# Kernel optimization log

Hardware: AMD Instinct MI355X
Metric: run time of the kernel (lower is better)

The kernel has to match this reference:

```python
import jax, jax.numpy as jnp
import numpy as np

B, S, D_IN, D_OUT = 4, 2048, 1024, 1024

def setup_inputs() -> dict:
    key = jax.random.key(0)
    k1, k2, k3, k4 = jax.random.split(key, 4)
    x = jax.random.normal(k1, (B, S, D_IN), dtype=jnp.float32)
    # nn.Linear(d_in, d_out, bias=False): y = x @ W.T with W [d_out, d_in].
    # We store the transposed [d_in, d_out] matrices directly.
    Wq = jax.random.normal(k2, (D_IN, D_OUT), dtype=jnp.float32) * (1.0 / np.sqrt(D_IN))
    Wk = jax.random.normal(k3, (D_IN, D_OUT), dtype=jnp.float32) * (1.0 / np.sqrt(D_IN))
    Wv = jax.random.normal(k4, (D_IN, D_OUT), dtype=jnp.float32) * (1.0 / np.sqrt(D_IN))
    return {"x": x, "Wq": Wq, "Wk": Wk, "Wv": Wv}

def reference(x, Wq, Wk, Wv):
    b, num_tokens, d_in = x.shape
    q = jnp.einsum('bsd,de->bse', x, Wq)
    k = jnp.einsum('bsd,de->bse', x, Wk)
    v = jnp.einsum('bsd,de->bse', x, Wv)
    scale = 1.0 / jnp.sqrt(jnp.asarray(k.shape[-1], dtype=x.dtype))
    scores = jnp.einsum('bqe,bke->bqk', q, k)  # [b, S, S]
    causal = jnp.tril(jnp.ones((num_tokens, num_tokens), dtype=bool))
    scores = jnp.where(causal[None, :, :], scores, -jnp.inf)
    attn = jax.nn.softmax(scores * scale, axis=-1)
    # dropout p=0.0 (eval/deterministic): identity
    return jnp.einsum('bqk,bke->bqe', attn, v)
```

## Files before the change

### kernel.cpp

```cpp
#include <hip/hip_runtime.h>

typedef unsigned short u16;
typedef unsigned int u32;
typedef __attribute__((ext_vector_type(8))) __bf16 bf16x8;
typedef __attribute__((ext_vector_type(4))) float f32x4;
typedef __attribute__((ext_vector_type(4))) u16 u16x4;

#define DEVFN static __device__ __forceinline__

constexpr int S_ = 2048;
constexpr int D_ = 1024;
constexpr float SCALE_ = 0.03125f;

DEVFN u16 f2bf(float f) {
  u32 u = __builtin_bit_cast(u32, f);
  return (u16)((u + 0x7fffu + ((u >> 16) & 1u)) >> 16);
}
DEVFN float bf2f(u16 h) {
  u32 u = ((u32)h) << 16;
  return __builtin_bit_cast(float, u);
}
DEVFN void gld16(const u16* g, u16* l) {
  __builtin_amdgcn_global_load_lds(
      (const __attribute__((address_space(1))) u32*)g,
      (__attribute__((address_space(3))) u32*)l, 16, 0, 0);
}

__global__ __launch_bounds__(256) void cvt_x_kernel(const float* __restrict__ x,
                                                    u16* __restrict__ xb) {
  int i = blockIdx.x * 256 + threadIdx.x;
  float4 v = ((const float4*)x)[i];
  u16x4 o = {f2bf(v.x), f2bf(v.y), f2bf(v.z), f2bf(v.w)};
  ((u16x4*)xb)[i] = o;
}

__global__ __launch_bounds__(256) void transpose_w_kernel(const float* __restrict__ W,
                                                          u16* __restrict__ Wt) {
  __shared__ float t[32][33];
  int tx = threadIdx.x, ty = threadIdx.y;
  int n0 = blockIdx.x * 32, k0 = blockIdx.y * 32;
#pragma unroll
  for (int i = 0; i < 4; ++i)
    t[ty + i * 8][tx] = W[(size_t)(k0 + ty + i * 8) * D_ + n0 + tx];
  __syncthreads();
#pragma unroll
  for (int i = 0; i < 4; ++i)
    Wt[(size_t)(n0 + ty + i * 8) * D_ + k0 + tx] = f2bf(t[tx][ty + i * 8]);
}

__global__ __launch_bounds__(256) void reduce_mt_kernel(const float* __restrict__ P4,
                                                        u16* __restrict__ Mt) {
  int i = (blockIdx.x * 256 + threadIdx.x) * 4;
  float4 a = *(const float4*)(P4 + i);
  float4 b = *(const float4*)(P4 + 1048576 + i);
  float4 c = *(const float4*)(P4 + 2097152 + i);
  float4 d = *(const float4*)(P4 + 3145728 + i);
  u16x4 o = {f2bf(a.x + b.x + c.x + d.x), f2bf(a.y + b.y + c.y + d.y),
             f2bf(a.z + b.z + c.z + d.z), f2bf(a.w + b.w + c.w + d.w)};
  *(u16x4*)(Mt + i) = o;
}

__global__ __launch_bounds__(512, 2) void gemm256(const u16* __restrict__ A,
                                                  const u16* __restrict__ Bt,
                                                  u16* __restrict__ O0,
                                                  u16* __restrict__ O2) {
  int tm = blockIdx.x, tn = blockIdx.y;
  constexpr int LDA = 1024, LDB = 1024;
  const int NKT = 32;

  __shared__ u16 ls[4][2][8192];

  int tid = threadIdx.x;
  int lane = tid & 63, wid = tid >> 6;
  int wm = wid >> 2, wn = wid & 3;

  const u16* Ab = A + (size_t)tm * 256 * LDA;
  const u16* Bb = Bt + (size_t)tn * 256 * LDB;

  int gsw = tid ^ ((tid >> 3) & 7);
  int srow = gsw >> 2;
  int scol = (gsw & 3) * 8;

#define STAGE(bf, kt)                                                           \
  do {                                                                          \
    int k0_ = (kt) * 32;                                                        \
    gld16(Ab + (size_t)srow * LDA + k0_ + scol, &ls[bf][0][0] + tid * 8);       \
    gld16(Ab + (size_t)(srow + 128) * LDA + k0_ + scol,                         \
          &ls[bf][0][0] + 4096 + tid * 8);                                      \
    gld16(Bb + (size_t)srow * LDB + k0_ + scol, &ls[bf][1][0] + tid * 8);       \
    gld16(Bb + (size_t)(srow + 128) * LDB + k0_ + scol,                         \
          &ls[bf][1][0] + 4096 + tid * 8);                                      \
  } while (0)

  const int kg_ = lane >> 4;
  const int arow = wm * 128 + (lane & 15);
  const int brow = wn * 64 + (lane & 15);
  const int aoff = ((arow * 4 + kg_) ^ ((arow >> 1) & 7)) * 8;
  const int boff = ((brow * 4 + kg_) ^ ((brow >> 1) & 7)) * 8;

  f32x4 acc[8][4] = {};

  STAGE(0, 0);
  STAGE(1, 1);
  STAGE(2, 2);

#define KSTEP(t, W)                                                             \
  do {                                                                          \
    asm volatile("s_waitcnt vmcnt(%0)" ::"n"(W) : "memory");                    \
    __builtin_amdgcn_s_barrier();                                               \
    __builtin_amdgcn_sched_barrier(0);                                          \
    if ((t) + 3 < NKT) STAGE(((t) + 3) & 3, (t) + 3);                           \
    const u16* la_ = &ls[(t) & 3][0][0] + aoff;                                 \
    const u16* lb_ = &ls[(t) & 3][1][0] + boff;                                 \
    bf16x8 aF[8], bF[4];                                                        \
    _Pragma("unroll") for (int f = 0; f < 8; ++f)                               \
        aF[f] = *(const bf16x8*)(la_ + f * 512);                                \
    _Pragma("unroll") for (int f = 0; f < 4; ++f)                               \
        bF[f] = *(const bf16x8*)(lb_ + f * 512);                                \
    __builtin_amdgcn_s_setprio(1);                                              \
    _Pragma("unroll") for (int fm = 0; fm < 8; ++fm)                            \
        _Pragma("unroll") for (int fn = 0; fn < 4; ++fn)                        \
            acc[fm][fn] = __builtin_amdgcn_mfma_f32_16x16x32_bf16(              \
                aF[fm], bF[fn], acc[fm][fn], 0, 0, 0);                          \
    __builtin_amdgcn_s_setprio(0);                                              \
  } while (0)

  for (int t = 0; t < NKT - 2; ++t) KSTEP(t, 8);
  KSTEP(NKT - 2, 4);
  KSTEP(NKT - 1, 0);

#undef KSTEP
#undef STAGE

  int r0 = tm * 256 + wm * 128 + (lane >> 4) * 4;
  int c0 = tn * 256 + wn * 64 + (lane & 15);

  if (tn < 4) {
#pragma unroll
    for (int fm = 0; fm < 8; ++fm)
#pragma unroll
      for (int fn = 0; fn < 4; ++fn)
#pragma unroll
        for (int i = 0; i < 4; ++i)
          O0[(size_t)(r0 + fm * 16 + i) * 1024 + (c0 + fn * 16)] =
              f2bf(acc[fm][fn][i]);
  } else {
#pragma unroll
    for (int fm = 0; fm < 8; ++fm)
#pragma unroll
      for (int fn = 0; fn < 4; ++fn) {
        int r = r0 + fm * 16;
        int bb = r >> 11, s0 = r & 2047;
        int e = c0 + fn * 16 - 1024;
        u16x4 o = {f2bf(acc[fm][fn][0]), f2bf(acc[fm][fn][1]),
                   f2bf(acc[fm][fn][2]), f2bf(acc[fm][fn][3])};
        *(u16x4*)(O2 + (size_t)bb * 2097152 + (size_t)e * 2048 + s0) = o;
      }
  }
}

template <int MODE, int NBUF>
__global__ __launch_bounds__(256, NBUF == 3 ? 3 : 2) void
gemm128(const u16* __restrict__ A, const u16* __restrict__ Bt,
        u16* __restrict__ O0, float* __restrict__ OF) {
  int tm, tn, z;
  if (MODE == 3) {
    int id = blockIdx.x;
    tn = id & 7;
    z = (id >> 3) & 3;
    int tmh = id >> 5;
    tm = (tmh < 8) ? tmh : 23 - tmh;
  } else if (MODE == 2) {
    int id = blockIdx.x;
    z = id & 3;
    int tri = id >> 2;
    int r = (int)((sqrtf(8.0f * (float)tri + 1.0f) - 1.0f) * 0.5f);
    while ((r + 1) * (r + 2) / 2 <= tri) ++r;
    while (r * (r + 1) / 2 > tri) --r;
    tm = r;
    tn = tri - r * (r + 1) / 2;
  } else {
    tm = blockIdx.x;
    tn = blockIdx.y;
    z = blockIdx.z;
  }
  constexpr int LDA = (MODE == 3) ? 2048 : 1024;
  constexpr int LDB = (MODE == 3) ? 2048 : 1024;
  const int NKT = (MODE == 3) ? (tm + 1) * 4 : (MODE == 4 ? 8 : 32);

  __shared__ u16 ls[NBUF][2][4096];

  int tid = threadIdx.x;
  int lane = tid & 63, wid = tid >> 6;
  int wm = wid >> 1, wn = wid & 1;

  const u16* Ab = A +
      (MODE == 2 ? (size_t)z * (2048 * 1024)
                 : (MODE == 3 ? (size_t)z * (2048 * 2048) : (size_t)0)) +
      (MODE == 4 ? z * 256 : 0) + (size_t)tm * 128 * LDA;
  const u16* Bb = Bt +
      (MODE == 2 ? (size_t)z * (2048 * 1024)
                 : (MODE == 3 ? (size_t)z * (1024 * 2048) : (size_t)0)) +
      (MODE == 4 ? z * 256 : 0) + (size_t)tn * 128 * LDB;

  int gsw = tid ^ ((tid >> 3) & 7);
  int sr = gsw >> 2;
  int sc = (gsw & 3) * 8;

#define STG(bf, kt)                                                             \
  do {                                                                          \
    int k0_ = (kt) * 32;                                                        \
    gld16(Ab + (size_t)sr * LDA + k0_ + sc, &ls[bf][0][0] + tid * 8);           \
    gld16(Ab + (size_t)(sr + 64) * LDA + k0_ + sc,                              \
          &ls[bf][0][0] + 2048 + tid * 8);                                      \
    gld16(Bb + (size_t)sr * LDB + k0_ + sc, &ls[bf][1][0] + tid * 8);           \
    gld16(Bb + (size_t)(sr + 64) * LDB + k0_ + sc,                              \
          &ls[bf][1][0] + 2048 + tid * 8);                                      \
  } while (0)

  const int kg_ = lane >> 4;
  const int arow = wm * 64 + (lane & 15);
  const int brow = wn * 64 + (lane & 15);
  const int aoff = ((arow * 4 + kg_) ^ ((arow >> 1) & 7)) * 8;
  const int boff = ((brow * 4 + kg_) ^ ((brow >> 1) & 7)) * 8;

  f32x4 acc[4][4] = {};
  int rb = 0, wb = 2;

  STG(0, 0);
  STG(1, 1);
  if (NBUF == 4) STG(2, 2);

#define KSTEP(t, W)                                                             \
  do {                                                                          \
    asm volatile("s_waitcnt vmcnt(%0)" ::"n"(W) : "memory");                    \
    __builtin_amdgcn_s_barrier();                                               \
    __builtin_amdgcn_sched_barrier(0);                                          \
    if (NBUF == 4) {                                                            \
      if ((t) + 3 < NKT) STG(((t) + 3) & 3, (t) + 3);                           \
    } else {                                                                    \
      if ((t) + 2 < NKT) STG(wb, (t) + 2);                                      \
    }                                                                           \
    const u16* la_ = &ls[(NBUF == 4) ? ((t) & 3) : rb][0][0] + aoff;            \
    const u16* lb_ = &ls[(NBUF == 4) ? ((t) & 3) : rb][1][0] + boff;            \
    bf16x8 aF[4], bF[4];                                                        \
    _Pragma("unroll") for (int f = 0; f < 4; ++f)                               \
        aF[f] = *(const bf16x8*)(la_ + f * 512);                                \
    _Pragma("unroll") for (int f = 0; f < 4; ++f)                               \
        bF[f] = *(const bf16x8*)(lb_ + f * 512);                                \
    __builtin_amdgcn_s_setprio(1);                                              \
    _Pragma("unroll") for (int fm = 0; fm < 4; ++fm)                            \
        _Pragma("unroll") for (int fn = 0; fn < 4; ++fn)                        \
            acc[fm][fn] = __builtin_amdgcn_mfma_f32_16x16x32_bf16(              \
                aF[fm], bF[fn], acc[fm][fn], 0, 0, 0);                          \
    __builtin_amdgcn_s_setprio(0);                                              \
    if (NBUF == 3) {                                                            \
      rb = (rb == 2) ? 0 : rb + 1;                                              \
      wb = (wb == 2) ? 0 : wb + 1;                                              \
    }                                                                           \
  } while (0)

  if (NBUF == 4) {
    for (int t = 0; t < NKT - 2; ++t) KSTEP(t, 8);
    KSTEP(NKT - 2, 4);
    KSTEP(NKT - 1, 0);
  } else {
    for (int t = 0; t < NKT - 1; ++t) KSTEP(t, 4);
    KSTEP(NKT - 1, 0);
  }

#undef KSTEP
#undef STG

  int r0 = tm * 128 + wm * 64 + (lane >> 4) * 4;
  int c0 = tn * 128 + wn * 64 + (lane & 15);

  if (MODE == 2) {
    u16* P = O0 + (size_t)z * 4194304;
#pragma unroll
    for (int fm = 0; fm < 4; ++fm)
#pragma unroll
      for (int fn = 0; fn < 4; ++fn)
#pragma unroll
        for (int i = 0; i < 4; ++i)
          P[(size_t)(r0 + fm * 16 + i) * 2048 + (c0 + fn * 16)] =
              f2bf(acc[fm][fn][i]);
  } else if (MODE == 4) {
    float* Ob = OF + (size_t)z * 1048576;
#pragma unroll
    for (int fm = 0; fm < 4; ++fm)
#pragma unroll
      for (int fn = 0; fn < 4; ++fn)
#pragma unroll
        for (int i = 0; i < 4; ++i)
          Ob[(size_t)(r0 + fm * 16 + i) * 1024 + (c0 + fn * 16)] = acc[fm][fn][i];
  } else {
    float* Ob = OF + (size_t)z * 2097152;
#pragma unroll
    for (int fm = 0; fm < 4; ++fm)
#pragma unroll
      for (int fn = 0; fn < 4; ++fn)
#pragma unroll
        for (int i = 0; i < 4; ++i)
          Ob[(size_t)(r0 + fm * 16 + i) * 1024 + (c0 + fn * 16)] = acc[fm][fn][i];
  }
}

__global__ __launch_bounds__(256) void softmax_causal_kernel(u16* __restrict__ P) {
  int wid = threadIdx.x >> 6, lane = threadIdx.x & 63;
  int row = blockIdx.x * 4 + wid;
  int b = row >> 11, q = row & 2047;
  int nit = (q >> 7) + 1;
  u16* rp = P + ((size_t)b * S_ + q) * S_;

  float vals[32];
  float m = -1e30f;
#pragma unroll
  for (int it = 0; it < 16; ++it)
    if (it < nit) {
      int s0 = it * 128 + lane * 2;
      u32 u = *(const u32*)(rp + s0);
      float v0 = bf2f((u16)u) * SCALE_;
      float v1 = bf2f((u16)(u >> 16)) * SCALE_;
      v0 = (s0 <= q) ? v0 : -1e30f;
      v1 = (s0 + 1 <= q) ? v1 : -1e30f;
      vals[2 * it] = v0;
      vals[2 * it + 1] = v1;
      m = fmaxf(m, fmaxf(v0, v1));
    }
#pragma unroll
  for (int off = 32; off; off >>= 1) m = fmaxf(m, __shfl_xor(m, off, 64));

  float l = 0.f;
#pragma unroll
  for (int it = 0; it < 16; ++it)
    if (it < nit) {
      vals[2 * it] = __expf(vals[2 * it] - m);
      vals[2 * it + 1] = __expf(vals[2 * it + 1] - m);
      l += vals[2 * it] + vals[2 * it + 1];
    }
#pragma unroll
  for (int off = 32; off; off >>= 1) l += __shfl_xor(l, off, 64);
  float inv = 1.0f / l;

#pragma unroll
  for (int it = 0; it < 16; ++it)
    if (it < nit) {
      int s0 = it * 128 + lane * 2;
      u32 o = (u32)f2bf(vals[2 * it] * inv) |
              ((u32)f2bf(vals[2 * it + 1] * inv) << 16);
      *(u32*)(rp + s0) = o;
    }
}

extern "C" void kernel_launch(void* const* d_in, const int* in_sizes, int n_in,
                              void* d_out, int out_size, void* d_ws, size_t ws_size,
                              hipStream_t stream) {
  const float* x = (const float*)d_in[0];
  const float* Wq = (const float*)d_in[1];
  const float* Wk = (const float*)d_in[2];
  const float* Wv = (const float*)d_in[3];
  float* out = (float*)d_out;

  u16* ws = (u16*)d_ws;
  u16* Xb = ws;
  u16* Xt = ws + 8388608;
  u16* Wqb = ws + 16777216;
  u16* Wkb = ws + 17825792;
  u16* Vt = ws + 25165824;
  u16* Pm = ws + 33554432;
  float* Pp = (float*)(ws + 33554432);
  u16* Wcat = ws + 50331648;
  u16* Mt = Wcat;
  u16* Wvt = Wcat + 1048576;

  cvt_x_kernel<<<8192, 256, 0, stream>>>(x, Xb);
  cvt_x_kernel<<<1024, 256, 0, stream>>>(Wq, Wqb);
  cvt_x_kernel<<<1024, 256, 0, stream>>>(Wk, Wkb);
  transpose_w_kernel<<<dim3(32, 32), dim3(32, 8), 0, stream>>>(Wv, Wvt);

  gemm128<4, 4><<<dim3(8, 8, 4), 256, 0, stream>>>(Wkb, Wqb, nullptr, Pp);
  reduce_mt_kernel<<<1024, 256, 0, stream>>>(Pp, Mt);

  gemm256<<<dim3(32, 8), 512, 0, stream>>>(Xb, Wcat, Xt, Vt);

  gemm128<2, 3><<<dim3(544, 1, 1), 256, 0, stream>>>(Xt, Xb, Pm, nullptr);

  softmax_causal_kernel<<<2048, 256, 0, stream>>>(Pm);

  gemm128<3, 4><<<dim3(512, 1, 1), 256, 0, stream>>>(Pm, Vt, nullptr, out);
}
```

Baseline: 140.0 us.

## Restructure gemm256 into double-buffered 64-wide K tiles with four-phase interleaved MFMA

Replaces the 4-stage, 32-wide-K pipeline of the projection GEMM with a 2-stage double buffer holding 64-wide K tiles. Each K step is split into four quadrant phases, and each phase interleaves LDS fragment reads, partial global-to-LDS prefetches and MFMA groups separated by barriers. The goal is to hide LDS and global load latency behind matrix-core work and to halve the number of outer iterations. In exchange it adds more barriers per step, uses a new LDS swizzle layout, and keeps only one tile of prefetch lookahead.

```diff
diff --git a/kernel.cpp b/kernel.cpp
--- a/kernel.cpp
+++ b/kernel.cpp
@@ -60,77 +60,141 @@
   *(u16x4*)(Mt + i) = o;
 }
 
-__global__ __launch_bounds__(512, 2) void gemm256(const u16* __restrict__ A,
-                                                  const u16* __restrict__ Bt,
-                                                  u16* __restrict__ O0,
-                                                  u16* __restrict__ O2) {
+__global__ __launch_bounds__(512, 2) void gemm256_8p(const u16* __restrict__ A,
+                                                     const u16* __restrict__ Bt,
+                                                     u16* __restrict__ O0,
+                                                     u16* __restrict__ O2) {
   int tm = blockIdx.x, tn = blockIdx.y;
-  constexpr int LDA = 1024, LDB = 1024;
-  const int NKT = 32;
-
-  __shared__ u16 ls[4][2][8192];
+  constexpr int LD = 1024;
+  constexpr int NKT = 16;
+
+  __shared__ u16 lsA[2][16384];
+  __shared__ u16 lsB[2][16384];
 
   int tid = threadIdx.x;
   int lane = tid & 63, wid = tid >> 6;
   int wm = wid >> 2, wn = wid & 3;
 
-  const u16* Ab = A + (size_t)tm * 256 * LDA;
-  const u16* Bb = Bt + (size_t)tn * 256 * LDB;
+  const u16* Ab = A + (size_t)tm * 256 * LD;
+  const u16* Bb = Bt + (size_t)tn * 256 * LD;
 
   int gsw = tid ^ ((tid >> 3) & 7);
-  int srow = gsw >> 2;
-  int scol = (gsw & 3) * 8;
-
-#define STAGE(bf, kt)                                                           \
-  do {                                                                          \
-    int k0_ = (kt) * 32;                                                        \
-    gld16(Ab + (size_t)srow * LDA + k0_ + scol, &ls[bf][0][0] + tid * 8);       \
-    gld16(Ab + (size_t)(srow + 128) * LDA + k0_ + scol,                         \
-          &ls[bf][0][0] + 4096 + tid * 8);                                      \
-    gld16(Bb + (size_t)srow * LDB + k0_ + scol, &ls[bf][1][0] + tid * 8);       \
-    gld16(Bb + (size_t)(srow + 128) * LDB + k0_ + scol,                         \
-          &ls[bf][1][0] + 4096 + tid * 8);                                      \
-  } while (0)
-
-  const int kg_ = lane >> 4;
+  int grow = gsw >> 3;
+  int gcol = (gsw & 7) * 8;
+
+#define STG_A(bf, q, kt)                                                        \
+  gld16(Ab + (size_t)((q)*64 + grow) * LD + (kt)*64 + gcol,                     \
+        &lsA[bf][(q)*4096 + tid * 8])
+#define STG_B(bf, q, kt)                                                        \
+  gld16(Bb + (size_t)((q)*64 + grow) * LD + (kt)*64 + gcol,                     \
+        &lsB[bf][(q)*4096 + tid * 8])
+
+  const int kg = lane >> 4;
+  const int sw = lane & 7;
   const int arow = wm * 128 + (lane & 15);
   const int brow = wn * 64 + (lane & 15);
-  const int aoff = ((arow * 4 + kg_) ^ ((arow >> 1) & 7)) * 8;
-  const int boff = ((brow * 4 + kg_) ^ ((brow >> 1) & 7)) * 8;
+  const int a0 = arow * 64 + ((kg ^ sw) * 8);
+  const int a1 = arow * 64 + (((kg + 4) ^ sw) * 8);
+  const int b0 = brow * 64 + ((kg ^ sw) * 8);
+  const int b1 = brow * 64 + (((kg + 4) ^ sw) * 8);
 
   f32x4 acc[8][4] = {};
-
-  STAGE(0, 0);
-  STAGE(1, 1);
-  STAGE(2, 2);
-
-#define KSTEP(t, W)                                                             \
+  bf16x8 aF[4][2], bQ0[2][2], bQ1[2][2];
+
+#pragma unroll
+  for (int q = 0; q < 4; ++q) { STG_A(0, q, 0); STG_B(0, q, 0); }
+#pragma unroll
+  for (int q = 0; q < 4; ++q) { STG_A(1, q, 1); STG_B(1, q, 1); }
+
+#define MM(fm, fn, AF, BF)                                                      \
+  acc[fm][fn] = __builtin_amdgcn_mfma_f32_16x16x32_bf16(AF, BF, acc[fm][fn], 0, 0, 0)
+
+#define KT_BODY(kt, W, ST)                                                      \
   do {                                                                          \
+    const int bf_ = (kt) & 1;                                                   \
+    const u16* la_ = &lsA[bf_][0];                                              \
+    const u16* lb_ = &lsB[bf_][0];                                              \
+          \
     asm volatile("s_waitcnt vmcnt(%0)" ::"n"(W) : "memory");                    \
     __builtin_amdgcn_s_barrier();                                               \
     __builtin_amdgcn_sched_barrier(0);                                          \
-    if ((t) + 3 < NKT) STAGE(((t) + 3) & 3, (t) + 3);                           \
-    const u16* la_ = &ls[(t) & 3][0][0] + aoff;                                 \
-    const u16* lb_ = &ls[(t) & 3][1][0] + boff;                                 \
-    bf16x8 aF[8], bF[4];                                                        \
-    _Pragma("unroll") for (int f = 0; f < 8; ++f)                               \
-        aF[f] = *(const bf16x8*)(la_ + f * 512);                                \
-    _Pragma("unroll") for (int f = 0; f < 4; ++f)                               \
-        bF[f] = *(const bf16x8*)(lb_ + f * 512);                                \
+    _Pragma("unroll") for (int fm = 0; fm < 4; ++fm) {                          \
+      aF[fm][0] = *(const bf16x8*)(la_ + a0 + fm * 1024);                       \
+      aF[fm][1] = *(const bf16x8*)(la_ + a1 + fm * 1024);                       \
+    }                                                                           \
+    _Pragma("unroll") for (int fn = 0; fn < 2; ++fn) {                          \
+      bQ0[fn][0] = *(const bf16x8*)(lb_ + b0 + fn * 1024);                      \
+      bQ0[fn][1] = *(const bf16x8*)(lb_ + b1 + fn * 1024);                      \
+    }                                                                           \
+    asm volatile("s_waitcnt lgkmcnt(0)" ::: "memory");                          \
+    __builtin_amdgcn_sched_barrier(0);                                          \
     __builtin_amdgcn_s_setprio(1);                                              \
-    _Pragma("unroll") for (int fm = 0; fm < 8; ++fm)                            \
-        _Pragma("unroll") for (int fn = 0; fn < 4; ++fn)                        \
-            acc[fm][fn] = __builtin_amdgcn_mfma_f32_16x16x32_bf16(              \
-                aF[fm], bF[fn], acc[fm][fn], 0, 0, 0);                          \
+    _Pragma("unroll") for (int fm = 0; fm < 4; ++fm)                            \
+        _Pragma("unroll") for (int fn = 0; fn < 2; ++fn) {                      \
+      MM(fm, fn, aF[fm][0], bQ0[fn][0]);                                        \
+      MM(fm, fn, aF[fm][1], bQ0[fn][1]);                                        \
+    }                                                                           \
     __builtin_amdgcn_s_setprio(0);                                              \
+    __builtin_amdgcn_s_barrier();                                               \
+    __builtin_amdgcn_sched_barrier(0);                                          \
+           \
+    _Pragma("unroll") for (int fn = 0; fn < 2; ++fn) {                          \
+      bQ1[fn][0] = *(const bf16x8*)(lb_ + b0 + (fn + 2) * 1024);                \
+      bQ1[fn][1] = *(const bf16x8*)(lb_ + b1 + (fn + 2) * 1024);                \
+    }                                                                           \
+    if (ST) { STG_A(bf_, 0, (kt) + 2); STG_A(bf_, 2, (kt) + 2); }               \
+    asm volatile("s_waitcnt lgkmcnt(0)" ::: "memory");                          \
+    __builtin_amdgcn_sched_barrier(0);                                          \
+    __builtin_amdgcn_s_setprio(1);                                              \
+    _Pragma("unroll") for (int fm = 0; fm < 4; ++fm)                            \
+        _Pragma("unroll") for (int fn = 0; fn < 2; ++fn) {                      \
+      MM(fm, fn + 2, aF[fm][0], bQ1[fn][0]);                                    \
+      MM(fm, fn + 2, aF[fm][1], bQ1[fn][1]);                                    \
+    }                                                                           \
+    __builtin_amdgcn_s_setprio(0);                                              \
+    __builtin_amdgcn_s_barrier();                                               \
+    __builtin_amdgcn_sched_barrier(0);                                          \
+                   \
+    _Pragma("unroll") for (int fm = 0; fm < 4; ++fm) {                          \
+      aF[fm][0] = *(const bf16x8*)(la_ + a0 + (fm + 4) * 1024);                 \
+      aF[fm][1] = *(const bf16x8*)(la_ + a1 + (fm + 4) * 1024);                 \
+    }                                                                           \
+    if (ST) { STG_B(bf_, 0, (kt) + 2); STG_B(bf_, 1, (kt) + 2); }               \
+    asm volatile("s_waitcnt lgkmcnt(0)" ::: "memory");                          \
+    __builtin_amdgcn_sched_barrier(0);                                          \
+    __builtin_amdgcn_s_setprio(1);                                              \
+    _Pragma("unroll") for (int fm = 0; fm < 4; ++fm)                            \
+        _Pragma("unroll") for (int fn = 0; fn < 2; ++fn) {                      \
+      MM(fm + 4, fn + 2, aF[fm][0], bQ1[fn][0]);                                \
+      MM(fm + 4, fn + 2, aF[fm][1], bQ1[fn][1]);                                \
+    }                                                                           \
+    __builtin_amdgcn_s_setprio(0);                                              \
+    __builtin_amdgcn_s_barrier();                                               \
+    __builtin_amdgcn_sched_barrier(0);                                          \
+       \
+    if (ST) {                                                                   \
+      STG_B(bf_, 2, (kt) + 2); STG_B(bf_, 3, (kt) + 2);                         \
+      STG_A(bf_, 1, (kt) + 2); STG_A(bf_, 3, (kt) + 2);                         \
+    }                                                                           \
+    __builtin_amdgcn_sched_barrier(0);                                          \
+    __builtin_amdgcn_s_setprio(1);                                              \
+    _Pragma("unroll") for (int fm = 0; fm < 4; ++fm)                            \
+        _Pragma("unroll") for (int fn = 0; fn < 2; ++fn) {                      \
+      MM(fm + 4, fn, aF[fm][0], bQ0[fn][0]);                                    \
+      MM(fm + 4, fn, aF[fm][1], bQ0[fn][1]);                                    \
+    }                                                                           \
+    __builtin_amdgcn_s_setprio(0);                                              \
+                  \
   } while (0)
 
-  for (int t = 0; t < NKT - 2; ++t) KSTEP(t, 8);
-  KSTEP(NKT - 2, 4);
-  KSTEP(NKT - 1, 0);
-
-#undef KSTEP
-#undef STAGE
+  for (int kt = 0; kt < NKT - 2; ++kt) KT_BODY(kt, 8, true);
+  KT_BODY(NKT - 2, 8, false);
+  KT_BODY(NKT - 1, 0, false);
+
+#undef KT_BODY
+#undef MM
+#undef STG_A
+#undef STG_B
 
   int r0 = tm * 256 + wm * 128 + (lane >> 4) * 4;
   int c0 = tn * 256 + wn * 64 + (lane & 15);
@@ -382,7 +446,7 @@
   gemm128<4, 4><<<dim3(8, 8, 4), 256, 0, stream>>>(Wkb, Wqb, nullptr, Pp);
   reduce_mt_kernel<<<1024, 256, 0, stream>>>(Pp, Mt);
 
-  gemm256<<<dim3(32, 8), 512, 0, stream>>>(Xb, Wcat, Xt, Vt);
+  gemm256_8p<<<dim3(32, 8), 512, 0, stream>>>(Xb, Wcat, Xt, Vt);
 
   gemm128<2, 3><<<dim3(544, 1, 1), 256, 0, stream>>>(Xt, Xb, Pm, nullptr);
 
```

Result: no change. 142.4 us (+1.8%).

## Fuse softmax into score GEMM epilogue and PV GEMM prologue via partial stats

Applied to the files above, without the earlier changes.

Removes the standalone causal softmax pass over the score matrix. The QK^T GEMM epilogue now writes scaled scores and per-tile row max/sum partials. A small kernel merges those partials into per-row max and inverse sum. A new PV kernel exponentiates and normalizes the score tiles while staging them into shared memory, applying the causal mask on diagonal tiles. This saves a full read and write of the bf16 score matrix, but adds exp work inside the PV loop and routes the A operand through registers instead of direct-to-LDS loads.

```diff
diff --git a/kernel.cpp b/kernel.cpp
--- a/kernel.cpp
+++ b/kernel.cpp
@@ -162,15 +162,9 @@
 template <int MODE, int NBUF>
 __global__ __launch_bounds__(256, NBUF == 3 ? 3 : 2) void
 gemm128(const u16* __restrict__ A, const u16* __restrict__ Bt,
-        u16* __restrict__ O0, float* __restrict__ OF) {
+        u16* __restrict__ O0, float* __restrict__ OF, float2* __restrict__ SP) {
   int tm, tn, z;
-  if (MODE == 3) {
-    int id = blockIdx.x;
-    tn = id & 7;
-    z = (id >> 3) & 3;
-    int tmh = id >> 5;
-    tm = (tmh < 8) ? tmh : 23 - tmh;
-  } else if (MODE == 2) {
+  if (MODE == 2) {
     int id = blockIdx.x;
     z = id & 3;
     int tri = id >> 2;
@@ -184,9 +178,8 @@
     tn = blockIdx.y;
     z = blockIdx.z;
   }
-  constexpr int LDA = (MODE == 3) ? 2048 : 1024;
-  constexpr int LDB = (MODE == 3) ? 2048 : 1024;
-  const int NKT = (MODE == 3) ? (tm + 1) * 4 : (MODE == 4 ? 8 : 32);
+  constexpr int LDA = 1024, LDB = 1024;
+  const int NKT = (MODE == 4) ? 8 : 32;
 
   __shared__ u16 ls[NBUF][2][4096];
 
@@ -194,14 +187,10 @@
   int lane = tid & 63, wid = tid >> 6;
   int wm = wid >> 1, wn = wid & 1;
 
-  const u16* Ab = A +
-      (MODE == 2 ? (size_t)z * (2048 * 1024)
-                 : (MODE == 3 ? (size_t)z * (2048 * 2048) : (size_t)0)) +
-      (MODE == 4 ? z * 256 : 0) + (size_t)tm * 128 * LDA;
-  const u16* Bb = Bt +
-      (MODE == 2 ? (size_t)z * (2048 * 1024)
-                 : (MODE == 3 ? (size_t)z * (1024 * 2048) : (size_t)0)) +
-      (MODE == 4 ? z * 256 : 0) + (size_t)tn * 128 * LDB;
+  const u16* Ab = A + (MODE == 2 ? (size_t)z * (2048 * 1024) : (size_t)0) +
+                  (MODE == 4 ? z * 256 : 0) + (size_t)tm * 128 * LDA;
+  const u16* Bb = Bt + (MODE == 2 ? (size_t)z * (2048 * 1024) : (size_t)0) +
+                  (MODE == 4 ? z * 256 : 0) + (size_t)tn * 128 * LDB;
 
   int gsw = tid ^ ((tid >> 3) & 7);
   int sr = gsw >> 2;
@@ -284,18 +273,43 @@
 #pragma unroll
         for (int i = 0; i < 4; ++i)
           P[(size_t)(r0 + fm * 16 + i) * 2048 + (c0 + fn * 16)] =
-              f2bf(acc[fm][fn][i]);
-  } else if (MODE == 4) {
+              f2bf(acc[fm][fn][i] * SCALE_);
+    float2* sst = (float2*)&ls[0][0][0];
+    int g16 = lane & 15;
+#pragma unroll
+    for (int fm = 0; fm < 4; ++fm)
+#pragma unroll
+      for (int i = 0; i < 4; ++i) {
+        int rg = r0 + fm * 16 + i;
+        float vv[4];
+        float mv = -1e30f;
+#pragma unroll
+        for (int fn = 0; fn < 4; ++fn) {
+          int cg = c0 + fn * 16;
+          float v = acc[fm][fn][i] * SCALE_;
+          v = (cg <= rg) ? v : -1e30f;
+          vv[fn] = v;
+          mv = fmaxf(mv, v);
+        }
+#pragma unroll
+        for (int off = 1; off < 16; off <<= 1)
+          mv = fmaxf(mv, __shfl_xor(mv, off, 64));
+        float lv = 0.f;
+#pragma unroll
+        for (int fn = 0; fn < 4; ++fn) lv += __expf(vv[fn] - mv);
+#pragma unroll
+        for (int off = 1; off < 16; off <<= 1) lv += __shfl_xor(lv, off, 64);
+        if (g16 == 0) sst[(rg - tm * 128) * 2 + wn] = make_float2(mv, lv);
+      }
+    __syncthreads();
+    if (tid < 128) {
+      float2 a = sst[tid * 2], b = sst[tid * 2 + 1];
+      float M = fmaxf(a.x, b.x);
+      float L = a.y * __expf(a.x - M) + b.y * __expf(b.x - M);
+      SP[((size_t)z * 2048 + tm * 128 + tid) * 16 + tn] = make_float2(M, L);
+    }
+  } else {
     float* Ob = OF + (size_t)z * 1048576;
-#pragma unroll
-    for (int fm = 0; fm < 4; ++fm)
-#pragma unroll
-      for (int fn = 0; fn < 4; ++fn)
-#pragma unroll
-        for (int i = 0; i < 4; ++i)
-          Ob[(size_t)(r0 + fm * 16 + i) * 1024 + (c0 + fn * 16)] = acc[fm][fn][i];
-  } else {
-    float* Ob = OF + (size_t)z * 2097152;
 #pragma unroll
     for (int fm = 0; fm < 4; ++fm)
 #pragma unroll
@@ -306,51 +320,154 @@
   }
 }
 
-__global__ __launch_bounds__(256) void softmax_causal_kernel(u16* __restrict__ P) {
-  int wid = threadIdx.x >> 6, lane = threadIdx.x & 63;
-  int row = blockIdx.x * 4 + wid;
-  int b = row >> 11, q = row & 2047;
-  int nit = (q >> 7) + 1;
-  u16* rp = P + ((size_t)b * S_ + q) * S_;
-
-  float vals[32];
-  float m = -1e30f;
-#pragma unroll
-  for (int it = 0; it < 16; ++it)
-    if (it < nit) {
-      int s0 = it * 128 + lane * 2;
-      u32 u = *(const u32*)(rp + s0);
-      float v0 = bf2f((u16)u) * SCALE_;
-      float v1 = bf2f((u16)(u >> 16)) * SCALE_;
-      v0 = (s0 <= q) ? v0 : -1e30f;
-      v1 = (s0 + 1 <= q) ? v1 : -1e30f;
-      vals[2 * it] = v0;
-      vals[2 * it + 1] = v1;
-      m = fmaxf(m, fmaxf(v0, v1));
-    }
-#pragma unroll
-  for (int off = 32; off; off >>= 1) m = fmaxf(m, __shfl_xor(m, off, 64));
-
-  float l = 0.f;
-#pragma unroll
-  for (int it = 0; it < 16; ++it)
-    if (it < nit) {
-      vals[2 * it] = __expf(vals[2 * it] - m);
-      vals[2 * it + 1] = __expf(vals[2 * it + 1] - m);
-      l += vals[2 * it] + vals[2 * it + 1];
-    }
-#pragma unroll
-  for (int off = 32; off; off >>= 1) l += __shfl_xor(l, off, 64);
-  float inv = 1.0f / l;
-
-#pragma unroll
-  for (int it = 0; it < 16; ++it)
-    if (it < nit) {
-      int s0 = it * 128 + lane * 2;
-      u32 o = (u32)f2bf(vals[2 * it] * inv) |
-              ((u32)f2bf(vals[2 * it + 1] * inv) << 16);
-      *(u32*)(rp + s0) = o;
-    }
+__global__ __launch_bounds__(256) void merge_stats_kernel(
+    const float2* __restrict__ SP, float2* __restrict__ ST) {
+  int idx = blockIdx.x * 256 + threadIdx.x;
+  int q = idx & 2047;
+  int nt = (q >> 7) + 1;
+  const float2* p = SP + (size_t)idx * 16;
+  float M = -1e30f;
+  for (int t = 0; t < nt; ++t) M = fmaxf(M, p[t].x);
+  float L = 0.f;
+  for (int t = 0; t < nt; ++t) L += p[t].y * __expf(p[t].x - M);
+  ST[idx] = make_float2(M, 1.0f / L);
+}
+
+__global__ __launch_bounds__(256, 3) void pv_fused(const u16* __restrict__ Pm,
+                                                   const u16* __restrict__ Vt,
+                                                   const float2* __restrict__ ST,
+                                                   float* __restrict__ out) {
+  int id = blockIdx.x;
+  int tn = id & 7;
+  int z = (id >> 3) & 3;
+  int tmh = id >> 5;
+  int tm = (tmh < 8) ? tmh : 23 - tmh;
+  const int NKT = (tm + 1) * 4;
+
+  __shared__ u16 Al[2][4096];
+  __shared__ u16 Vl[4][4096];
+
+  int tid = threadIdx.x;
+  int lane = tid & 63, wid = tid >> 6;
+  int wm = wid >> 1, wn = wid & 1;
+
+  const u16* Ab = Pm + (size_t)z * (2048 * 2048) + (size_t)tm * 128 * 2048;
+  const u16* Bb = Vt + (size_t)z * (1024 * 2048) + (size_t)tn * 128 * 2048;
+
+  int gsw = tid ^ ((tid >> 3) & 7);
+  int sr = gsw >> 2;
+  int sc = (gsw & 3) * 8;
+
+  int q0 = tm * 128 + sr, q1 = q0 + 64;
+  float2 st0 = ST[z * 2048 + q0];
+  float2 st1 = ST[z * 2048 + q1];
+
+  const int kg_ = lane >> 4;
+  const int arow = wm * 64 + (lane & 15);
+  const int brow = wn * 64 + (lane & 15);
+  const int aoff = ((arow * 4 + kg_) ^ ((arow >> 1) & 7)) * 8;
+  const int boff = ((brow * 4 + kg_) ^ ((brow >> 1) & 7)) * 8;
+
+  f32x4 acc[4][4] = {};
+  uint4 rA0, rA1, rB0, rB1;
+
+#define ALOAD(R0, R1, kt)                                                      \
+  do {                                                                         \
+    R0 = *(const uint4*)(Ab + (size_t)sr * 2048 + (kt) * 32 + sc);             \
+    R1 = *(const uint4*)(Ab + (size_t)(sr + 64) * 2048 + (kt) * 32 + sc);      \
+  } while (0)
+#define VGLD(bf, kt)                                                           \
+  do {                                                                         \
+    gld16(Bb + (size_t)sr * 2048 + (kt) * 32 + sc, &Vl[bf][0] + tid * 8);      \
+    gld16(Bb + (size_t)(sr + 64) * 2048 + (kt) * 32 + sc,                      \
+          &Vl[bf][0] + 2048 + tid * 8);                                        \
+  } while (0)
+#define EXPWRITE(R0, R1, buf, kt)                                              \
+  do {                                                                         \
+    int kb = (kt) * 32 + sc;                                                   \
+    bool dm = (kt) >= NKT - 4;                                                 \
+    u32 w[4];                                                                  \
+    const u32* pr = (const u32*)&R0;                                           \
+    _Pragma("unroll") for (int h = 0; h < 4; ++h) {                            \
+      float p0 = __expf(bf2f((u16)pr[h]) - st0.x) * st0.y;                     \
+      float p1 = __expf(bf2f((u16)(pr[h] >> 16)) - st0.x) * st0.y;             \
+      if (dm) {                                                                \
+        if (kb + 2 * h > q0) p0 = 0.f;                                         \
+        if (kb + 2 * h + 1 > q0) p1 = 0.f;                                     \
+      }                                                                        \
+      w[h] = (u32)f2bf(p0) | ((u32)f2bf(p1) << 16);                            \
+    }                                                                          \
+    *(uint4*)(&Al[buf][0] + tid * 8) = *(const uint4*)w;                       \
+    pr = (const u32*)&R1;                                                      \
+    _Pragma("unroll") for (int h = 0; h < 4; ++h) {                            \
+      float p0 = __expf(bf2f((u16)pr[h]) - st1.x) * st1.y;                     \
+      float p1 = __expf(bf2f((u16)(pr[h] >> 16)) - st1.x) * st1.y;             \
+      if (dm) {                                                                \
+        if (kb + 2 * h > q1) p0 = 0.f;                                         \
+        if (kb + 2 * h + 1 > q1) p1 = 0.f;                                     \
+      }                                                                        \
+      w[h] = (u32)f2bf(p0) | ((u32)f2bf(p1) << 16);                            \
+    }                                                                          \
+    *(uint4*)(&Al[buf][0] + 2048 + tid * 8) = *(const uint4*)w;                \
+  } while (0)
+
+  ALOAD(rA0, rA1, 0);
+  EXPWRITE(rA0, rA1, 0, 0);
+  VGLD(0, 0);
+  ALOAD(rB0, rB1, 1);
+  VGLD(1, 1);
+  asm volatile("s_waitcnt lgkmcnt(0)" ::: "memory");
+
+#define PV_ITER(t, E0, E1, L0, L1)                                             \
+  do {                                                                         \
+    if ((t) == NKT - 1)                                                        \
+      asm volatile("s_waitcnt vmcnt(0)" ::: "memory");                         \
+    else                                                                       \
+      asm volatile("s_waitcnt vmcnt(2)" ::: "memory");                         \
+    __builtin_amdgcn_s_barrier();                                              \
+    __builtin_amdgcn_sched_barrier(0);                                         \
+    const u16* la_ = &Al[(t) & 1][0] + aoff;                                   \
+    const u16* lb_ = &Vl[(t) & 3][0] + boff;                                   \
+    bf16x8 aF[4], bF[4];                                                       \
+    _Pragma("unroll") for (int f = 0; f < 4; ++f) {                            \
+      aF[f] = *(const bf16x8*)(la_ + f * 512);                                 \
+      bF[f] = *(const bf16x8*)(lb_ + f * 512);                                 \
+    }                                                                          \
+    if ((t) + 1 < NKT) EXPWRITE(E0, E1, ((t) + 1) & 1, (t) + 1);               \
+    if ((t) + 2 < NKT) {                                                       \
+      ALOAD(L0, L1, (t) + 2);                                                  \
+      VGLD(((t) + 2) & 3, (t) + 2);                                            \
+    }                                                                          \
+    asm volatile("s_waitcnt lgkmcnt(0)" ::: "memory");                         \
+    __builtin_amdgcn_sched_barrier(0);                                         \
+    __builtin_amdgcn_s_setprio(1);                                             \
+    _Pragma("unroll") for (int fm = 0; fm < 4; ++fm)                           \
+        _Pragma("unroll") for (int fn = 0; fn < 4; ++fn)                       \
+            acc[fm][fn] = __builtin_amdgcn_mfma_f32_16x16x32_bf16(             \
+                aF[fm], bF[fn], acc[fm][fn], 0, 0, 0);                         \
+    __builtin_amdgcn_s_setprio(0);                                             \
+  } while (0)
+
+  for (int t = 0; t < NKT; t += 2) {
+    PV_ITER(t, rB0, rB1, rA0, rA1);
+    PV_ITER(t + 1, rA0, rA1, rB0, rB1);
+  }
+
+#undef PV_ITER
+#undef EXPWRITE
+#undef VGLD
+#undef ALOAD
+
+  int r0 = tm * 128 + wm * 64 + (lane >> 4) * 4;
+  int c0 = tn * 128 + wn * 64 + (lane & 15);
+  float* Ob = out + (size_t)z * 2097152;
+#pragma unroll
+  for (int fm = 0; fm < 4; ++fm)
+#pragma unroll
+    for (int fn = 0; fn < 4; ++fn)
+#pragma unroll
+      for (int i = 0; i < 4; ++i)
+        Ob[(size_t)(r0 + fm * 16 + i) * 1024 + (c0 + fn * 16)] = acc[fm][fn][i];
 }
 
 extern "C" void kernel_launch(void* const* d_in, const int* in_sizes, int n_in,
@@ -373,20 +490,22 @@
   u16* Wcat = ws + 50331648;
   u16* Mt = Wcat;
   u16* Wvt = Wcat + 1048576;
+  float2* SP = (float2*)(ws + 52428800);
+  float2* ST = (float2*)(ws + 52953088);
 
   cvt_x_kernel<<<8192, 256, 0, stream>>>(x, Xb);
   cvt_x_kernel<<<1024, 256, 0, stream>>>(Wq, Wqb);
   cvt_x_kernel<<<1024, 256, 0, stream>>>(Wk, Wkb);
   transpose_w_kernel<<<dim3(32, 32), dim3(32, 8), 0, stream>>>(Wv, Wvt);
 
-  gemm128<4, 4><<<dim3(8, 8, 4), 256, 0, stream>>>(Wkb, Wqb, nullptr, Pp);
+  gemm128<4, 4><<<dim3(8, 8, 4), 256, 0, stream>>>(Wkb, Wqb, nullptr, Pp, nullptr);
   reduce_mt_kernel<<<1024, 256, 0, stream>>>(Pp, Mt);
 
   gemm256<<<dim3(32, 8), 512, 0, stream>>>(Xb, Wcat, Xt, Vt);
 
-  gemm128<2, 3><<<dim3(544, 1, 1), 256, 0, stream>>>(Xt, Xb, Pm, nullptr);
-
-  softmax_causal_kernel<<<2048, 256, 0, stream>>>(Pm);
-
-  gemm128<3, 4><<<dim3(512, 1, 1), 256, 0, stream>>>(Pm, Vt, nullptr, out);
-}
+  gemm128<2, 3><<<dim3(544, 1, 1), 256, 0, stream>>>(Xt, Xb, Pm, nullptr, SP);
+
+  merge_stats_kernel<<<32, 256, 0, stream>>>(SP, ST);
+
+  pv_fused<<<dim3(512, 1, 1), 256, 0, stream>>>(Pm, Vt, ST, out);
+}
```

After: 173.9 us. 1.24x slower.

## Restructure 256x256 projection GEMM into an 8-phase pipeline with K=64 tiles

Applied to the files above, without the earlier changes.

Rewrites the fused X@[M|Wv] GEMM main loop to use 64-wide K tiles split into half-tile LDS buffers. Each tile is processed in four phases that interleave fragment loads, async global->LDS staging of the next half-tile, barriers and MFMA batches. The goal is finer overlap of memory and compute with fewer loop iterations. The cost is more barriers per tile, a new LDS swizzle and more complex buffer-reuse ordering, which raises correctness and register-pressure risk.

```diff
diff --git a/kernel.cpp b/kernel.cpp
--- a/kernel.cpp
+++ b/kernel.cpp
@@ -60,77 +60,136 @@
   *(u16x4*)(Mt + i) = o;
 }
 
-__global__ __launch_bounds__(512, 2) void gemm256(const u16* __restrict__ A,
-                                                  const u16* __restrict__ Bt,
-                                                  u16* __restrict__ O0,
-                                                  u16* __restrict__ O2) {
+__global__ __launch_bounds__(512, 2) void gemm256_8p(const u16* __restrict__ A,
+                                                     const u16* __restrict__ Bt,
+                                                     u16* __restrict__ O0,
+                                                     u16* __restrict__ O2) {
   int tm = blockIdx.x, tn = blockIdx.y;
-  constexpr int LDA = 1024, LDB = 1024;
-  const int NKT = 32;
-
-  __shared__ u16 ls[4][2][8192];
+  constexpr int NKT = 16;
+
+  __shared__ u16 lsA[4][8192];
+  __shared__ u16 lsB[4][8192];
 
   int tid = threadIdx.x;
   int lane = tid & 63, wid = tid >> 6;
   int wm = wid >> 2, wn = wid & 3;
 
-  const u16* Ab = A + (size_t)tm * 256 * LDA;
-  const u16* Bb = Bt + (size_t)tn * 256 * LDB;
+  const u16* Ab = A + (size_t)tm * 256 * 1024;
+  const u16* Bb = Bt + (size_t)tn * 256 * 1024;
 
   int gsw = tid ^ ((tid >> 3) & 7);
-  int srow = gsw >> 2;
-  int scol = (gsw & 3) * 8;
-
-#define STAGE(bf, kt)                                                           \
+  int grow = gsw >> 3;
+  int gcol = (gsw & 7) * 8;
+
+#define STGA(t, h)                                                              \
   do {                                                                          \
-    int k0_ = (kt) * 32;                                                        \
-    gld16(Ab + (size_t)srow * LDA + k0_ + scol, &ls[bf][0][0] + tid * 8);       \
-    gld16(Ab + (size_t)(srow + 128) * LDA + k0_ + scol,                         \
-          &ls[bf][0][0] + 4096 + tid * 8);                                      \
-    gld16(Bb + (size_t)srow * LDB + k0_ + scol, &ls[bf][1][0] + tid * 8);       \
-    gld16(Bb + (size_t)(srow + 128) * LDB + k0_ + scol,                         \
-          &ls[bf][1][0] + 4096 + tid * 8);                                      \
+    const u16* s_ = Ab + (size_t)((h)*128 + grow) * 1024 + (t)*64 + gcol;       \
+    u16* d_ = &lsA[(2 * (t) + (h)) & 3][0] + tid * 8;                           \
+    gld16(s_, d_);                                                              \
+    gld16(s_ + 65536, d_ + 4096);                                               \
   } while (0)
-
-  const int kg_ = lane >> 4;
-  const int arow = wm * 128 + (lane & 15);
-  const int brow = wn * 64 + (lane & 15);
-  const int aoff = ((arow * 4 + kg_) ^ ((arow >> 1) & 7)) * 8;
-  const int boff = ((brow * 4 + kg_) ^ ((brow >> 1) & 7)) * 8;
+#define STGB(t, h)                                                              \
+  do {                                                                          \
+    const u16* s_ = Bb + (size_t)((h)*128 + grow) * 1024 + (t)*64 + gcol;       \
+    u16* d_ = &lsB[(2 * (t) + (h)) & 3][0] + tid * 8;                           \
+    gld16(s_, d_);                                                              \
+    gld16(s_ + 65536, d_ + 4096);                                               \
+  } while (0)
+
+  const int kg = lane >> 4;
+  const int cs0 = kg ^ (lane & 7);
+  const int aO0 = (lane & 15) * 64 + cs0 * 8;
+  const int aO1 = (lane & 15) * 64 + (cs0 ^ 4) * 8;
+  const int rb_ = (wn & 1) * 64 + (lane & 15);
+  const int bO0 = rb_ * 64 + cs0 * 8;
+  const int bO1 = rb_ * 64 + (cs0 ^ 4) * 8;
 
   f32x4 acc[8][4] = {};
-
-  STAGE(0, 0);
-  STAGE(1, 1);
-  STAGE(2, 2);
-
-#define KSTEP(t, W)                                                             \
-  do {                                                                          \
-    asm volatile("s_waitcnt vmcnt(%0)" ::"n"(W) : "memory");                    \
-    __builtin_amdgcn_s_barrier();                                               \
-    __builtin_amdgcn_sched_barrier(0);                                          \
-    if ((t) + 3 < NKT) STAGE(((t) + 3) & 3, (t) + 3);                           \
-    const u16* la_ = &ls[(t) & 3][0][0] + aoff;                                 \
-    const u16* lb_ = &ls[(t) & 3][1][0] + boff;                                 \
-    bf16x8 aF[8], bF[4];                                                        \
-    _Pragma("unroll") for (int f = 0; f < 8; ++f)                               \
-        aF[f] = *(const bf16x8*)(la_ + f * 512);                                \
-    _Pragma("unroll") for (int f = 0; f < 4; ++f)                               \
-        bF[f] = *(const bf16x8*)(lb_ + f * 512);                                \
-    __builtin_amdgcn_s_setprio(1);                                              \
-    _Pragma("unroll") for (int fm = 0; fm < 8; ++fm)                            \
-        _Pragma("unroll") for (int fn = 0; fn < 4; ++fn)                        \
-            acc[fm][fn] = __builtin_amdgcn_mfma_f32_16x16x32_bf16(              \
-                aF[fm], bF[fn], acc[fm][fn], 0, 0, 0);                          \
-    __builtin_amdgcn_s_setprio(0);                                              \
-  } while (0)
-
-  for (int t = 0; t < NKT - 2; ++t) KSTEP(t, 8);
-  KSTEP(NKT - 2, 4);
-  KSTEP(NKT - 1, 0);
-
-#undef KSTEP
-#undef STAGE
+  bf16x8 aFa[4], aFb[4], bF0[4], bF1[4];
+
+#define MM(FM, FN, AF, BF)                                                      \
+  acc[FM][FN] = __builtin_amdgcn_mfma_f32_16x16x32_bf16(AF, BF, acc[FM][FN], 0, 0, 0)
+
+  STGB(0, 0);
+  STGB(0, 1);
+  STGA(0, 0);
+  STGA(0, 1);
+  STGB(1, 0);
+  asm volatile("s_waitcnt vmcnt(2)" ::: "memory");
+  __builtin_amdgcn_s_barrier();
+  __builtin_amdgcn_sched_barrier(0);
+
+#pragma unroll 2
+  for (int T = 0; T < NKT; ++T) {
+    const u16* la = &lsA[(2 * T + wm) & 3][0];
+    const u16* lb = &lsB[(2 * T + (wn >> 1)) & 3][0];
+#pragma unroll
+    for (int f = 0; f < 4; ++f) {
+      aFa[f] = *(const bf16x8*)(la + aO0 + f * 1024);
+      bF0[f] = *(const bf16x8*)(lb + bO0 + f * 1024);
+    }
+    if (T + 1 < NKT) STGB(T + 1, 1);
+    __builtin_amdgcn_sched_barrier(0);
+    __builtin_amdgcn_s_barrier();
+    __builtin_amdgcn_sched_barrier(0);
+    __builtin_amdgcn_s_setprio(1);
+#pragma unroll
+    for (int fm = 0; fm < 4; ++fm)
+#pragma unroll
+      for (int fn = 0; fn < 4; ++fn) MM(fm, fn, aFa[fm], bF0[fn]);
+    __builtin_amdgcn_s_setprio(0);
+#pragma unroll
+    for (int f = 0; f < 4; ++f)
+      aFb[f] = *(const bf16x8*)(la + aO0 + (f + 4) * 1024);
+    if (T + 1 < NKT) STGA(T + 1, 1);
+    __builtin_amdgcn_sched_barrier(0);
+    __builtin_amdgcn_s_barrier();
+    __builtin_amdgcn_sched_barrier(0);
+    __builtin_amdgcn_s_setprio(1);
+#pragma unroll
+    for (int fm = 0; fm < 4; ++fm)
+#pragma unroll
+      for (int fn = 0; fn < 4; ++fn) MM(fm + 4, fn, aFb[fm], bF0[fn]);
+    __builtin_amdgcn_s_setprio(0);
+#pragma unroll
+    for (int f = 0; f < 4; ++f) {
+      aFa[f] = *(const bf16x8*)(la + aO1 + f * 1024);
+      bF1[f] = *(const bf16x8*)(lb + bO1 + f * 1024);
+    }
+    if (T + 1 < NKT) STGA(T + 1, 0);
+    __builtin_amdgcn_sched_barrier(0);
+    __builtin_amdgcn_s_barrier();
+    __builtin_amdgcn_sched_barrier(0);
+    __builtin_amdgcn_s_setprio(1);
+#pragma unroll
+    for (int fm = 0; fm < 4; ++fm)
+#pragma unroll
+      for (int fn = 0; fn < 4; ++fn) MM(fm, fn, aFa[fm], bF1[fn]);
+    __builtin_amdgcn_s_setprio(0);
+#pragma unroll
+    for (int f = 0; f < 4; ++f)
+      aFb[f] = *(const bf16x8*)(la + aO1 + (f + 4) * 1024);
+    if (T + 2 < NKT) {
+      STGB(T + 2, 0);
+      __builtin_amdgcn_sched_barrier(0);
+      asm volatile("s_waitcnt vmcnt(2)" ::: "memory");
+    } else {
+      __builtin_amdgcn_sched_barrier(0);
+      asm volatile("s_waitcnt vmcnt(0)" ::: "memory");
+    }
+    __builtin_amdgcn_s_barrier();
+    __builtin_amdgcn_sched_barrier(0);
+    __builtin_amdgcn_s_setprio(1);
+#pragma unroll
+    for (int fm = 0; fm < 4; ++fm)
+#pragma unroll
+      for (int fn = 0; fn < 4; ++fn) MM(fm + 4, fn, aFb[fm], bF1[fn]);
+    __builtin_amdgcn_s_setprio(0);
+  }
+
+#undef MM
+#undef STGA
+#undef STGB
 
   int r0 = tm * 256 + wm * 128 + (lane >> 4) * 4;
   int c0 = tn * 256 + wn * 64 + (lane & 15);
@@ -382,7 +441,7 @@
   gemm128<4, 4><<<dim3(8, 8, 4), 256, 0, stream>>>(Wkb, Wqb, nullptr, Pp);
   reduce_mt_kernel<<<1024, 256, 0, stream>>>(Pp, Mt);
 
-  gemm256<<<dim3(32, 8), 512, 0, stream>>>(Xb, Wcat, Xt, Vt);
+  gemm256_8p<<<dim3(32, 8), 512, 0, stream>>>(Xb, Wcat, Xt, Vt);
 
   gemm128<2, 3><<<dim3(544, 1, 1), 256, 0, stream>>>(Xt, Xb, Pm, nullptr);
 
```

Result: no change. 139.3 us (-0.5%).
